# Kernel optimization log

Hardware: AMD Instinct MI355X
Metric: run time of the kernel (lower is better)

The kernel has to match this reference:

```python
import math
import jax, jax.numpy as jnp
import numpy as np

N, T, F, H = 30000, 4, 128, 8  # num_node, num_type, num_fea, num_head
D = F // H


def setup_inputs() -> dict:
    key = jax.random.key(0)
    k0, k1, k2, k3, k4 = jax.random.split(key, 5)
    feature = jax.random.normal(k0, (N, F), dtype=jnp.float32)
    edge_fea = jax.random.normal(k1, (N, T, F), dtype=jnp.float32)
    node_multi_mask = jax.random.randint(k2, (N,), 0, T)
    # Xavier-uniform-like scale for [*, F, F] projection tables
    xav = math.sqrt(6.0 / (F + F))
    node_proj = jax.random.uniform(k3, (T, F, F), minval=-xav, maxval=xav, dtype=jnp.float32)
    edge_proj = jax.random.uniform(k4, (T * T, F, F), minval=-xav, maxval=xav, dtype=jnp.float32)
    return {
        "feature": feature,
        "edge_fea": edge_fea,
        "node_multi_mask": node_multi_mask,
        "node_proj": node_proj,
        "edge_proj": edge_proj,
    }


def reference(feature, edge_fea, node_multi_mask, node_proj, edge_proj):
    # Type-indexed projections. Instead of gathering per-node [F,F] matrices
    # (which would materialize N*F*F), compute projections for all T source
    # types in one batched einsum, then select each node's type with a gather.
    # node: out[n] = node_proj[mask[n]] @ feature[n]
    node_all = jnp.einsum('tgf,nf->ntg', node_proj, feature)           # [N,T,F]
    node_p = jnp.take_along_axis(node_all, node_multi_mask[:, None, None], axis=1)[:, 0]  # [N,F]
    # edge: out[n,j] = edge_proj[mask[n]*T + j] @ edge_fea[n,j]
    edge_proj_r = edge_proj.reshape(T, T, F, F)                         # [src_type, j, F, F]
    edge_all = jnp.einsum('stgf,ntf->nstg', edge_proj_r, edge_fea)      # [N,T_src,T,F]
    edge_p = jnp.take_along_axis(edge_all, node_multi_mask[:, None, None, None], axis=1)[:, 0]  # [N,T,F]

    # multi-head attention weights
    node_multi_in = node_p.reshape(N, 1, H, D).transpose(0, 2, 1, 3) / math.sqrt(D)  # [N,H,1,D]
    edge_multi_in = edge_p.reshape(N, T, H, D).transpose(0, 2, 3, 1)                  # [N,H,D,T]
    scores = jnp.matmul(node_multi_in, edge_multi_in)                                 # [N,H,1,T]
    # NOTE: original uses nn.Softmax(dim=1) -> softmax over the HEAD axis
    all_r_weight = jax.nn.softmax(scores, axis=1).transpose(0, 3, 1, 2)               # [N,T,H,1]
    return all_r_weight
```

## Files before the change

### kernel.cpp

```cpp
#include <hip/hip_runtime.h>
#include <hip/hip_bf16.h>

#define N_NODES 30000
#define T_TYPES 4
#define F_DIM   128
#define H_HEADS 8

typedef __bf16 bf16x8 __attribute__((ext_vector_type(8)));
typedef __bf16 bf16x4 __attribute__((ext_vector_type(4)));
typedef float  floatx4 __attribute__((ext_vector_type(4)));

#define WS_REORDER 64
#define WS_NPB     480256
#define WS_EPB     611328

template <int CTRL>
static __device__ __forceinline__ float dpp_add(float x) {
    int xi = __builtin_bit_cast(int, x);
    int yi = __builtin_amdgcn_update_dpp(xi, xi, CTRL, 0xF, 0xF, true);
    return x + __builtin_bit_cast(float, yi);
}
static __device__ __forceinline__ float sum16(float x) {
    x = dpp_add<0xB1>(x);
    x = dpp_add<0x4E>(x);
    x = dpp_add<0x141>(x);
    x = dpp_add<0x140>(x);
    return x;
}

__global__ __launch_bounds__(256) void prep_bucket_kernel(
    const float* __restrict__ node_proj, const float* __restrict__ edge_proj,
    const int* __restrict__ mask,
    __bf16* __restrict__ npb, __bf16* __restrict__ epb,
    int* __restrict__ counts, int* __restrict__ reorder)
{
    if (blockIdx.x < 320) {
        int i = blockIdx.x * 256 + threadIdx.x;
        int base = i * 4;
        float4 v;
        __bf16* dst;
        if (base < T_TYPES * F_DIM * F_DIM) {
            v = ((const float4*)node_proj)[i];
            dst = npb + base;
        } else {
            int off = base - T_TYPES * F_DIM * F_DIM;
            v = ((const float4*)edge_proj)[off >> 2];
            dst = epb + off;
        }
        bf16x4 w = { (__bf16)v.x, (__bf16)v.y, (__bf16)v.z, (__bf16)v.w };
        *(bf16x4*)dst = w;
    } else {
        int n = (blockIdx.x - 320) * 256 + threadIdx.x;
        int lane = threadIdx.x & 63;
        int t = (n < N_NODES) ? mask[n] : -1;
        #pragma unroll
        for (int tt = 0; tt < T_TYPES; ++tt) {
            unsigned long long b = __ballot(t == tt);
            if (b == 0ull) continue;
            int cnt = __popcll(b);
            int leader = __ffsll((unsigned long long)b) - 1;
            int base = 0;
            if (lane == leader) base = atomicAdd(&counts[tt], cnt);
            base = __shfl(base, leader);
            if (t == tt) {
                int prefix = __popcll(b & ((1ull << lane) - 1ull));
                reorder[tt * N_NODES + base + prefix] = n;
            }
        }
    }
}

__global__ __launch_bounds__(512, 8) void main_kernel(
    const float* __restrict__ feature, const float* __restrict__ edge_fea,
    const int* __restrict__ counts, const int* __restrict__ reorder,
    const __bf16* __restrict__ npb, const __bf16* __restrict__ epb,
    float* __restrict__ out)
{
    const int b = blockIdx.x;
    const int t = b & 3;
    const int start = (b >> 2) * 32;
    const int Nt = counts[t];
    if (start >= Nt) return;
    const int valid = min(32, Nt - start);

    __shared__ __bf16 Afeat[32][136];
    __shared__ __bf16 Aedge[2][32][136];
    __shared__ float  sc[32][4][H_HEADS];
    __shared__ int    nidx[32];

    const int tid = threadIdx.x;
    if (tid < 32) {
        int s = (tid < valid) ? tid : (valid - 1);
        nidx[tid] = reorder[t * N_NODES + start + s];
    }
    __syncthreads();

    const int colv = tid & 31;
    const int rowg = tid >> 5;
    const long nA = nidx[rowg], nB = nidx[rowg + 16];
    {
        float4 f0 = ((const float4*)(feature + nA * F_DIM))[colv];
        float4 f1 = ((const float4*)(feature + nB * F_DIM))[colv];
        float4 e0 = ((const float4*)(edge_fea + (nA * 4 + 0) * F_DIM))[colv];
        float4 e1 = ((const float4*)(edge_fea + (nB * 4 + 0) * F_DIM))[colv];
        bf16x4 w;
        w = (bf16x4){ (__bf16)f0.x, (__bf16)f0.y, (__bf16)f0.z, (__bf16)f0.w };
        *(bf16x4*)(&Afeat[rowg][0] + colv * 4) = w;
        w = (bf16x4){ (__bf16)f1.x, (__bf16)f1.y, (__bf16)f1.z, (__bf16)f1.w };
        *(bf16x4*)(&Afeat[rowg + 16][0] + colv * 4) = w;
        w = (bf16x4){ (__bf16)e0.x, (__bf16)e0.y, (__bf16)e0.z, (__bf16)e0.w };
        *(bf16x4*)(&Aedge[0][rowg][0] + colv * 4) = w;
        w = (bf16x4){ (__bf16)e1.x, (__bf16)e1.y, (__bf16)e1.z, (__bf16)e1.w };
        *(bf16x4*)(&Aedge[0][rowg + 16][0] + colv * 4) = w;
    }
    __syncthreads();

    const int lane = tid & 63;
    const int wave = tid >> 6;
    const int ml   = lane & 15;
    const int quad = lane >> 4;
    const int g0   = wave * 16;

    floatx4 accN[2] = {};
    {
        const __bf16* a0 = &Afeat[ml][quad * 8];
        const __bf16* a1 = &Afeat[16 + ml][quad * 8];
        const __bf16* b0 = npb + t * (F_DIM * F_DIM) + (g0 + ml) * F_DIM + quad * 8;
        #pragma unroll
        for (int k0 = 0; k0 < 128; k0 += 32) {
            bf16x8 A0 = *(const bf16x8*)(a0 + k0);
            bf16x8 A1 = *(const bf16x8*)(a1 + k0);
            bf16x8 B0 = *(const bf16x8*)(b0 + k0);
            accN[0] = __builtin_amdgcn_mfma_f32_16x16x32_bf16(A0, B0, accN[0], 0, 0, 0);
            accN[1] = __builtin_amdgcn_mfma_f32_16x16x32_bf16(A1, B0, accN[1], 0, 0, 0);
        }
    }

    #pragma unroll
    for (int j = 0; j < 4; ++j) {
        float4 e0, e1;
        if (j < 3) {
            e0 = ((const float4*)(edge_fea + (nA * 4 + j + 1) * F_DIM))[colv];
            e1 = ((const float4*)(edge_fea + (nB * 4 + j + 1) * F_DIM))[colv];
        }
        floatx4 accE[2] = {};
        {
            const __bf16* a0 = &Aedge[j & 1][ml][quad * 8];
            const __bf16* a1 = &Aedge[j & 1][16 + ml][quad * 8];
            const __bf16* b0 = epb + (t * 4 + j) * (F_DIM * F_DIM) + (g0 + ml) * F_DIM + quad * 8;
            #pragma unroll
            for (int k0 = 0; k0 < 128; k0 += 32) {
                bf16x8 A0 = *(const bf16x8*)(a0 + k0);
                bf16x8 A1 = *(const bf16x8*)(a1 + k0);
                bf16x8 B0 = *(const bf16x8*)(b0 + k0);
                accE[0] = __builtin_amdgcn_mfma_f32_16x16x32_bf16(A0, B0, accE[0], 0, 0, 0);
                accE[1] = __builtin_amdgcn_mfma_f32_16x16x32_bf16(A1, B0, accE[1], 0, 0, 0);
            }
        }
        #pragma unroll
        for (int mt = 0; mt < 2; ++mt) {
            floatx4 p = accN[mt] * accE[mt];
            p.x = sum16(p.x);
            p.y = sum16(p.y);
            p.z = sum16(p.z);
            p.w = sum16(p.w);
            if (ml == 0) {
                int mb = mt * 16 + quad * 4;
                sc[mb + 0][j][wave] = p.x * 0.25f;
                sc[mb + 1][j][wave] = p.y * 0.25f;
                sc[mb + 2][j][wave] = p.z * 0.25f;
                sc[mb + 3][j][wave] = p.w * 0.25f;
            }
        }
        if (j < 3) {
            bf16x4 w;
            w = (bf16x4){ (__bf16)e0.x, (__bf16)e0.y, (__bf16)e0.z, (__bf16)e0.w };
            *(bf16x4*)(&Aedge[(j + 1) & 1][rowg][0] + colv * 4) = w;
            w = (bf16x4){ (__bf16)e1.x, (__bf16)e1.y, (__bf16)e1.z, (__bf16)e1.w };
            *(bf16x4*)(&Aedge[(j + 1) & 1][rowg + 16][0] + colv * 4) = w;
        }
        __syncthreads();
    }

    if (tid < 128) {
        int node = tid >> 2, j = tid & 3;
        if (node < valid) {
            float v[8], m = -1e30f;
            #pragma unroll
            for (int h = 0; h < 8; ++h) { v[h] = sc[node][j][h]; m = fmaxf(m, v[h]); }
            float s = 0.f;
            #pragma unroll
            for (int h = 0; h < 8; ++h) { v[h] = __expf(v[h] - m); s += v[h]; }
            float r = 1.0f / s;
            float* o = out + (long)nidx[node] * (T_TYPES * H_HEADS) + j * H_HEADS;
            float4 o0 = { v[0] * r, v[1] * r, v[2] * r, v[3] * r };
            float4 o1 = { v[4] * r, v[5] * r, v[6] * r, v[7] * r };
            ((float4*)o)[0] = o0;
            ((float4*)o)[1] = o1;
        }
    }
}

extern "C" void kernel_launch(void* const* d_in, const int* in_sizes, int n_in,
                              void* d_out, int out_size, void* d_ws, size_t ws_size,
                              hipStream_t stream) {
    const float* feature   = (const float*)d_in[0];
    const float* edge_fea  = (const float*)d_in[1];
    const int*   mask      = (const int*)d_in[2];
    const float* node_proj = (const float*)d_in[3];
    const float* edge_proj = (const float*)d_in[4];
    float* out = (float*)d_out;

    char* ws = (char*)d_ws;
    int*    counts  = (int*)ws;
    int*    reorder = (int*)(ws + WS_REORDER);
    __bf16* npb     = (__bf16*)(ws + WS_NPB);
    __bf16* epb     = (__bf16*)(ws + WS_EPB);

    hipMemsetAsync(counts, 0, 4 * sizeof(int), stream);
    prep_bucket_kernel<<<320 + (N_NODES + 255) / 256, 256, 0, stream>>>(
        node_proj, edge_proj, mask, npb, epb, counts, reorder);
    int nblk = ((N_NODES + 31) / 32) * T_TYPES;
    main_kernel<<<nblk, 512, 0, stream>>>(feature, edge_fea, counts, reorder, npb, epb, out);
}
```

Before: 146.9 us.

## Fuse memset, prep and main kernels into one persistent cooperative kernel

Replaces the memset, the weight-conversion/bucketing kernel and the main MFMA kernel with a single cooperative persistent kernel. Grid-wide syncs separate the counter reset and bf16 weight conversion, the type bucketing, and a grid-stride tile loop. The aim is to remove launch overhead and inter-kernel gaps. In exchange it adds two grid syncs and calls an occupancy query on every launch. The loss of launch_bounds min-blocks could lower occupancy.

Measured after the change: 298.1 us. 103% more time.

```diff
diff --git a/kernel.cpp b/kernel.cpp
--- a/kernel.cpp
+++ b/kernel.cpp
@@ -1,10 +1,15 @@
 #include <hip/hip_runtime.h>
 #include <hip/hip_bf16.h>
+#include <hip/hip_cooperative_groups.h>
+
+namespace cg = cooperative_groups;
 
 #define N_NODES 30000
 #define T_TYPES 4
 #define F_DIM   128
 #define H_HEADS 8
+#define NTILES  (((N_NODES + 31) / 32) * T_TYPES)
+#define NCONV   81920
 
 typedef __bf16 bf16x8 __attribute__((ext_vector_type(8)));
 typedef __bf16 bf16x4 __attribute__((ext_vector_type(4)));
@@ -28,17 +33,28 @@
     return x;
 }
 
-__global__ __launch_bounds__(256) void prep_bucket_kernel(
+__global__ __launch_bounds__(512) void fused_kernel(
+    const float* __restrict__ feature, const float* __restrict__ edge_fea,
+    const int* __restrict__ mask,
     const float* __restrict__ node_proj, const float* __restrict__ edge_proj,
-    const int* __restrict__ mask,
+    int* __restrict__ counts, int* __restrict__ reorder,
     __bf16* __restrict__ npb, __bf16* __restrict__ epb,
-    int* __restrict__ counts, int* __restrict__ reorder)
+    float* __restrict__ out)
 {
-    if (blockIdx.x < 320) {
-        int i = blockIdx.x * 256 + threadIdx.x;
+    cg::grid_group gg = cg::this_grid();
+    const int tid   = threadIdx.x;
+    const int gtid  = blockIdx.x * 512 + tid;
+    const int gsize = gridDim.x * 512;
+
+    __shared__ __bf16 Afeat[32][136];
+    __shared__ __bf16 Aedge[2][32][136];
+    __shared__ float  sc[32][4][H_HEADS];
+    __shared__ int    nidx[32];
+
+    if (gtid < T_TYPES) counts[gtid] = 0;
+    for (int i = gtid; i < NCONV; i += gsize) {
         int base = i * 4;
-        float4 v;
-        __bf16* dst;
+        float4 v; __bf16* dst;
         if (base < T_TYPES * F_DIM * F_DIM) {
             v = ((const float4*)node_proj)[i];
             dst = npb + base;
@@ -49,155 +65,152 @@
         }
         bf16x4 w = { (__bf16)v.x, (__bf16)v.y, (__bf16)v.z, (__bf16)v.w };
         *(bf16x4*)dst = w;
-    } else {
-        int n = (blockIdx.x - 320) * 256 + threadIdx.x;
-        int lane = threadIdx.x & 63;
-        int t = (n < N_NODES) ? mask[n] : -1;
-        #pragma unroll
-        for (int tt = 0; tt < T_TYPES; ++tt) {
-            unsigned long long b = __ballot(t == tt);
-            if (b == 0ull) continue;
-            int cnt = __popcll(b);
-            int leader = __ffsll((unsigned long long)b) - 1;
-            int base = 0;
-            if (lane == leader) base = atomicAdd(&counts[tt], cnt);
-            base = __shfl(base, leader);
-            if (t == tt) {
-                int prefix = __popcll(b & ((1ull << lane) - 1ull));
-                reorder[tt * N_NODES + base + prefix] = n;
-            }
-        }
     }
-}
-
-__global__ __launch_bounds__(512, 8) void main_kernel(
-    const float* __restrict__ feature, const float* __restrict__ edge_fea,
-    const int* __restrict__ counts, const int* __restrict__ reorder,
-    const __bf16* __restrict__ npb, const __bf16* __restrict__ epb,
-    float* __restrict__ out)
-{
-    const int b = blockIdx.x;
-    const int t = b & 3;
-    const int start = (b >> 2) * 32;
-    const int Nt = counts[t];
-    if (start >= Nt) return;
-    const int valid = min(32, Nt - start);
-
-    __shared__ __bf16 Afeat[32][136];
-    __shared__ __bf16 Aedge[2][32][136];
-    __shared__ float  sc[32][4][H_HEADS];
-    __shared__ int    nidx[32];
-
-    const int tid = threadIdx.x;
-    if (tid < 32) {
-        int s = (tid < valid) ? tid : (valid - 1);
-        nidx[tid] = reorder[t * N_NODES + start + s];
+    __threadfence();
+    gg.sync();
+
+    {
+        const int lane = tid & 63;
+        const int nbound = ((N_NODES + 63) / 64) * 64;
+        for (int n = gtid; n < nbound; n += gsize) {
+            int t = (n < N_NODES) ? mask[n] : -1;
+            #pragma unroll
+            for (int tt = 0; tt < T_TYPES; ++tt) {
+                unsigned long long bm = __ballot(t == tt);
+                if (bm == 0ull) continue;
+                int cnt = __popcll(bm);
+                int leader = __ffsll(bm) - 1;
+                int base = 0;
+                if (lane == leader) base = atomicAdd(&counts[tt], cnt);
+                base = __shfl(base, leader);
+                if (t == tt) {
+                    int prefix = __popcll(bm & ((1ull << lane) - 1ull));
+                    reorder[tt * N_NODES + base + prefix] = n;
+                }
+            }
+        }
     }
-    __syncthreads();
-
-    const int colv = tid & 31;
-    const int rowg = tid >> 5;
-    const long nA = nidx[rowg], nB = nidx[rowg + 16];
-    {
-        float4 f0 = ((const float4*)(feature + nA * F_DIM))[colv];
-        float4 f1 = ((const float4*)(feature + nB * F_DIM))[colv];
-        float4 e0 = ((const float4*)(edge_fea + (nA * 4 + 0) * F_DIM))[colv];
-        float4 e1 = ((const float4*)(edge_fea + (nB * 4 + 0) * F_DIM))[colv];
-        bf16x4 w;
-        w = (bf16x4){ (__bf16)f0.x, (__bf16)f0.y, (__bf16)f0.z, (__bf16)f0.w };
-        *(bf16x4*)(&Afeat[rowg][0] + colv * 4) = w;
-        w = (bf16x4){ (__bf16)f1.x, (__bf16)f1.y, (__bf16)f1.z, (__bf16)f1.w };
-        *(bf16x4*)(&Afeat[rowg + 16][0] + colv * 4) = w;
-        w = (bf16x4){ (__bf16)e0.x, (__bf16)e0.y, (__bf16)e0.z, (__bf16)e0.w };
-        *(bf16x4*)(&Aedge[0][rowg][0] + colv * 4) = w;
-        w = (bf16x4){ (__bf16)e1.x, (__bf16)e1.y, (__bf16)e1.z, (__bf16)e1.w };
-        *(bf16x4*)(&Aedge[0][rowg + 16][0] + colv * 4) = w;
-    }
-    __syncthreads();
+    __threadfence();
+    gg.sync();
 
     const int lane = tid & 63;
     const int wave = tid >> 6;
     const int ml   = lane & 15;
     const int quad = lane >> 4;
     const int g0   = wave * 16;
-
-    floatx4 accN[2] = {};
-    {
-        const __bf16* a0 = &Afeat[ml][quad * 8];
-        const __bf16* a1 = &Afeat[16 + ml][quad * 8];
-        const __bf16* b0 = npb + t * (F_DIM * F_DIM) + (g0 + ml) * F_DIM + quad * 8;
-        #pragma unroll
-        for (int k0 = 0; k0 < 128; k0 += 32) {
-            bf16x8 A0 = *(const bf16x8*)(a0 + k0);
-            bf16x8 A1 = *(const bf16x8*)(a1 + k0);
-            bf16x8 B0 = *(const bf16x8*)(b0 + k0);
-            accN[0] = __builtin_amdgcn_mfma_f32_16x16x32_bf16(A0, B0, accN[0], 0, 0, 0);
-            accN[1] = __builtin_amdgcn_mfma_f32_16x16x32_bf16(A1, B0, accN[1], 0, 0, 0);
-        }
-    }
-
-    #pragma unroll
-    for (int j = 0; j < 4; ++j) {
-        float4 e0, e1;
-        if (j < 3) {
-            e0 = ((const float4*)(edge_fea + (nA * 4 + j + 1) * F_DIM))[colv];
-            e1 = ((const float4*)(edge_fea + (nB * 4 + j + 1) * F_DIM))[colv];
-        }
-        floatx4 accE[2] = {};
+    const int colv = tid & 31;
+    const int rowg = tid >> 5;
+
+    for (int tile = blockIdx.x; tile < NTILES; tile += gridDim.x) {
+        const int t = tile & 3;
+        const int start = (tile >> 2) * 32;
+        const int Nt = counts[t];
+        if (start >= Nt) continue;
+        const int valid = min(32, Nt - start);
+
+        if (tid < 32) {
+            int s = (tid < valid) ? tid : (valid - 1);
+            nidx[tid] = reorder[t * N_NODES + start + s];
+        }
+        __syncthreads();
+
+        const long nA = nidx[rowg], nB = nidx[rowg + 16];
         {
-            const __bf16* a0 = &Aedge[j & 1][ml][quad * 8];
-            const __bf16* a1 = &Aedge[j & 1][16 + ml][quad * 8];
-            const __bf16* b0 = epb + (t * 4 + j) * (F_DIM * F_DIM) + (g0 + ml) * F_DIM + quad * 8;
+            float4 f0 = ((const float4*)(feature + nA * F_DIM))[colv];
+            float4 f1 = ((const float4*)(feature + nB * F_DIM))[colv];
+            float4 e0 = ((const float4*)(edge_fea + (nA * 4 + 0) * F_DIM))[colv];
+            float4 e1 = ((const float4*)(edge_fea + (nB * 4 + 0) * F_DIM))[colv];
+            bf16x4 w;
+            w = (bf16x4){ (__bf16)f0.x, (__bf16)f0.y, (__bf16)f0.z, (__bf16)f0.w };
+            *(bf16x4*)(&Afeat[rowg][0] + colv * 4) = w;
+            w = (bf16x4){ (__bf16)f1.x, (__bf16)f1.y, (__bf16)f1.z, (__bf16)f1.w };
+            *(bf16x4*)(&Afeat[rowg + 16][0] + colv * 4) = w;
+            w = (bf16x4){ (__bf16)e0.x, (__bf16)e0.y, (__bf16)e0.z, (__bf16)e0.w };
+            *(bf16x4*)(&Aedge[0][rowg][0] + colv * 4) = w;
+            w = (bf16x4){ (__bf16)e1.x, (__bf16)e1.y, (__bf16)e1.z, (__bf16)e1.w };
+            *(bf16x4*)(&Aedge[0][rowg + 16][0] + colv * 4) = w;
+        }
+        __syncthreads();
+
+        floatx4 accN[2] = {};
+        {
+            const __bf16* a0 = &Afeat[ml][quad * 8];
+            const __bf16* a1 = &Afeat[16 + ml][quad * 8];
+            const __bf16* b0 = npb + t * (F_DIM * F_DIM) + (g0 + ml) * F_DIM + quad * 8;
             #pragma unroll
             for (int k0 = 0; k0 < 128; k0 += 32) {
                 bf16x8 A0 = *(const bf16x8*)(a0 + k0);
                 bf16x8 A1 = *(const bf16x8*)(a1 + k0);
                 bf16x8 B0 = *(const bf16x8*)(b0 + k0);
-                accE[0] = __builtin_amdgcn_mfma_f32_16x16x32_bf16(A0, B0, accE[0], 0, 0, 0);
-                accE[1] = __builtin_amdgcn_mfma_f32_16x16x32_bf16(A1, B0, accE[1], 0, 0, 0);
-            }
-        }
+                accN[0] = __builtin_amdgcn_mfma_f32_16x16x32_bf16(A0, B0, accN[0], 0, 0, 0);
+                accN[1] = __builtin_amdgcn_mfma_f32_16x16x32_bf16(A1, B0, accN[1], 0, 0, 0);
+            }
+        }
+
         #pragma unroll
-        for (int mt = 0; mt < 2; ++mt) {
-            floatx4 p = accN[mt] * accE[mt];
-            p.x = sum16(p.x);
-            p.y = sum16(p.y);
-            p.z = sum16(p.z);
-            p.w = sum16(p.w);
-            if (ml == 0) {
-                int mb = mt * 16 + quad * 4;
-                sc[mb + 0][j][wave] = p.x * 0.25f;
-                sc[mb + 1][j][wave] = p.y * 0.25f;
-                sc[mb + 2][j][wave] = p.z * 0.25f;
-                sc[mb + 3][j][wave] = p.w * 0.25f;
-            }
-        }
-        if (j < 3) {
-            bf16x4 w;
-            w = (bf16x4){ (__bf16)e0.x, (__bf16)e0.y, (__bf16)e0.z, (__bf16)e0.w };
-            *(bf16x4*)(&Aedge[(j + 1) & 1][rowg][0] + colv * 4) = w;
-            w = (bf16x4){ (__bf16)e1.x, (__bf16)e1.y, (__bf16)e1.z, (__bf16)e1.w };
-            *(bf16x4*)(&Aedge[(j + 1) & 1][rowg + 16][0] + colv * 4) = w;
+        for (int j = 0; j < 4; ++j) {
+            float4 e0, e1;
+            if (j < 3) {
+                e0 = ((const float4*)(edge_fea + (nA * 4 + j + 1) * F_DIM))[colv];
+                e1 = ((const float4*)(edge_fea + (nB * 4 + j + 1) * F_DIM))[colv];
+            }
+            floatx4 accE[2] = {};
+            {
+                const __bf16* a0 = &Aedge[j & 1][ml][quad * 8];
+                const __bf16* a1 = &Aedge[j & 1][16 + ml][quad * 8];
+                const __bf16* b0 = epb + (t * 4 + j) * (F_DIM * F_DIM) + (g0 + ml) * F_DIM + quad * 8;
+                #pragma unroll
+                for (int k0 = 0; k0 < 128; k0 += 32) {
+                    bf16x8 A0 = *(const bf16x8*)(a0 + k0);
+                    bf16x8 A1 = *(const bf16x8*)(a1 + k0);
+                    bf16x8 B0 = *(const bf16x8*)(b0 + k0);
+                    accE[0] = __builtin_amdgcn_mfma_f32_16x16x32_bf16(A0, B0, accE[0], 0, 0, 0);
+                    accE[1] = __builtin_amdgcn_mfma_f32_16x16x32_bf16(A1, B0, accE[1], 0, 0, 0);
+                }
+            }
+            #pragma unroll
+            for (int mt = 0; mt < 2; ++mt) {
+                floatx4 p = accN[mt] * accE[mt];
+                p.x = sum16(p.x);
+                p.y = sum16(p.y);
+                p.z = sum16(p.z);
+                p.w = sum16(p.w);
+                if (ml == 0) {
+                    int mb = mt * 16 + quad * 4;
+                    sc[mb + 0][j][wave] = p.x * 0.25f;
+                    sc[mb + 1][j][wave] = p.y * 0.25f;
+                    sc[mb + 2][j][wave] = p.z * 0.25f;
+                    sc[mb + 3][j][wave] = p.w * 0.25f;
+                }
+            }
+            if (j < 3) {
+                bf16x4 w;
+                w = (bf16x4){ (__bf16)e0.x, (__bf16)e0.y, (__bf16)e0.z, (__bf16)e0.w };
+                *(bf16x4*)(&Aedge[(j + 1) & 1][rowg][0] + colv * 4) = w;
+                w = (bf16x4){ (__bf16)e1.x, (__bf16)e1.y, (__bf16)e1.z, (__bf16)e1.w };
+                *(bf16x4*)(&Aedge[(j + 1) & 1][rowg + 16][0] + colv * 4) = w;
+            }
+            __syncthreads();
+        }
+
+        if (tid < 128) {
+            int node = tid >> 2, j = tid & 3;
+            if (node < valid) {
+                float v[8], m = -1e30f;
+                #pragma unroll
+                for (int h = 0; h < 8; ++h) { v[h] = sc[node][j][h]; m = fmaxf(m, v[h]); }
+                float s = 0.f;
+                #pragma unroll
+                for (int h = 0; h < 8; ++h) { v[h] = __expf(v[h] - m); s += v[h]; }
+                float r = 1.0f / s;
+                float* o = out + (long)nidx[node] * (T_TYPES * H_HEADS) + j * H_HEADS;
+                float4 o0 = { v[0] * r, v[1] * r, v[2] * r, v[3] * r };
+                float4 o1 = { v[4] * r, v[5] * r, v[6] * r, v[7] * r };
+                ((float4*)o)[0] = o0;
+                ((float4*)o)[1] = o1;
+            }
         }
         __syncthreads();
-    }
-
-    if (tid < 128) {
-        int node = tid >> 2, j = tid & 3;
-        if (node < valid) {
-            float v[8], m = -1e30f;
-            #pragma unroll
-            for (int h = 0; h < 8; ++h) { v[h] = sc[node][j][h]; m = fmaxf(m, v[h]); }
-            float s = 0.f;
-            #pragma unroll
-            for (int h = 0; h < 8; ++h) { v[h] = __expf(v[h] - m); s += v[h]; }
-            float r = 1.0f / s;
-            float* o = out + (long)nidx[node] * (T_TYPES * H_HEADS) + j * H_HEADS;
-            float4 o0 = { v[0] * r, v[1] * r, v[2] * r, v[3] * r };
-            float4 o1 = { v[4] * r, v[5] * r, v[6] * r, v[7] * r };
-            ((float4*)o)[0] = o0;
-            ((float4*)o)[1] = o1;
-        }
     }
 }
 
@@ -217,9 +230,14 @@
     __bf16* npb     = (__bf16*)(ws + WS_NPB);
     __bf16* epb     = (__bf16*)(ws + WS_EPB);
 
-    hipMemsetAsync(counts, 0, 4 * sizeof(int), stream);
-    prep_bucket_kernel<<<320 + (N_NODES + 255) / 256, 256, 0, stream>>>(
-        node_proj, edge_proj, mask, npb, epb, counts, reorder);
-    int nblk = ((N_NODES + 31) / 32) * T_TYPES;
-    main_kernel<<<nblk, 512, 0, stream>>>(feature, edge_fea, counts, reorder, npb, epb, out);
-}
+    int bpc = 0;
+    hipOccupancyMaxActiveBlocksPerMultiprocessor(&bpc, fused_kernel, 512, 0);
+    if (bpc < 1) bpc = 1;
+    unsigned G = (unsigned)bpc * 256u;
+    if (G > (unsigned)NTILES) G = (unsigned)NTILES;
+
+    void* args[] = { (void*)&feature, (void*)&edge_fea, (void*)&mask,
+                     (void*)&node_proj, (void*)&edge_proj, (void*)&counts,
+                     (void*)&reorder, (void*)&npb, (void*)&epb, (void*)&out };
+    hipLaunchCooperativeKernel(fused_kernel, dim3(G), dim3(512), args, 0, stream);
+}
```
